# Performance work log

Hardware: AMD Instinct MI355X
Metric: run time of the kernel (lower is better)

Reference implementation:

```python
import jax, jax.numpy as jnp
import numpy as np

NU, NI, K, D, B = 100000, 50000, 100, 64, 8192


def setup_inputs() -> dict:
    key = jax.random.key(0)
    ks = jax.random.split(key, 16)
    s = lambda fan_in: np.sqrt(2.0 / fan_in)  # kaiming_normal-ish scale
    return {
        "user_emb": jax.random.normal(ks[0], (NU, D), jnp.float32) * s(D),
        "item_emb": jax.random.normal(ks[1], (NI, D), jnp.float32) * s(D),
        "user_scr_tensor": jax.random.uniform(ks[2], (NU, K), jnp.float32) / K,
        "item_scr_tensor": jax.random.uniform(ks[3], (NI, K), jnp.float32) / K,
        "w1": jax.random.normal(ks[4], (64, 128), jnp.float32) * s(128),
        "b1": jnp.zeros((64,), jnp.float32),
        "w2": jax.random.normal(ks[5], (64, 64), jnp.float32) * s(64),
        "b2": jnp.zeros((64,), jnp.float32),
        "w3": jax.random.normal(ks[6], (32, 64), jnp.float32) * s(64),
        "b3": jnp.zeros((32,), jnp.float32),
        "w4": jax.random.normal(ks[7], (32, 32), jnp.float32) * s(32),
        "b4": jnp.zeros((32,), jnp.float32),
        "w5": jax.random.normal(ks[8], (1, 32), jnp.float32) * s(32),
        "b5": jnp.zeros((1,), jnp.float32),
        "user_idx_tensor": jax.random.randint(ks[9], (NU, K), 0, NU, jnp.int32),
        "item_idx_tensor": jax.random.randint(ks[10], (NI, K), 0, NI, jnp.int32),
        "user_idxs": jax.random.randint(ks[11], (B,), 0, NU, jnp.int32),
        "item_idxs": jax.random.randint(ks[12], (B,), 0, NI, jnp.int32),
    }


def _scored_pool(idx_tensor, emb, scr, idxs):
    neighs = idx_tensor[idxs]          # [B, K]
    neigh_emb = emb[neighs]            # [B, K, D]
    neigh_scr = scr[neighs]            # [B, K, K]
    return jnp.einsum("bkj,bjd->bkd", neigh_scr, neigh_emb)


def reference(user_emb, item_emb, user_scr_tensor, item_scr_tensor,
              w1, b1, w2, b2, w3, b3, w4, b4, w5, b5,
              user_idx_tensor, item_idx_tensor, user_idxs, item_idxs):
    su = _scored_pool(user_idx_tensor, user_emb, user_scr_tensor, user_idxs)  # [B,K,D]
    si = _scored_pool(item_idx_tensor, item_emb, item_scr_tensor, item_idxs)  # [B,K,D]
    x = jnp.concatenate([su, si], axis=2)  # [B, K, 2D]
    x = jax.nn.relu(x @ w1.T + b1)
    x = jax.nn.relu(x @ w2.T + b2)
    x = jax.nn.relu(x @ w3.T + b3)
    x = jax.nn.relu(x @ w4.T + b4)
    x = jax.nn.sigmoid(x @ w5.T + b5)  # [B, K, 1]
    return jnp.mean(x, axis=-2).squeeze()  # [B]
```

## Files before the change

kernel.cpp:

```cpp
#include <hip/hip_runtime.h>
#include <hip/hip_bf16.h>
#include <math.h>

typedef __attribute__((ext_vector_type(8))) short short8;
typedef __attribute__((ext_vector_type(4))) float f32x4;

#define KN 100

#define W1_OFF 0
#define W2_OFF 8192
#define W3_OFF 12288
#define W4_OFF 14336
#define SCRU_OFF 16384
#define SCRI_OFF (SCRU_OFF + 100000 * 128)
#define EMBU_OFF (SCRI_OFF + 50000 * 128)
#define EMBI_OFF (EMBU_OFF + 100000 * 64)

#define ET_STRIDE 136
#define S_TOT (64 * ET_STRIDE)

__device__ __forceinline__ unsigned short f2bf(float f) {
  __hip_bfloat16 h = __float2bfloat16(f);
  return __builtin_bit_cast(unsigned short, h);
}

__device__ __forceinline__ void st8(unsigned short* d, float4 a, float4 b) {
  short8 h;
  h[0] = (short)f2bf(a.x); h[1] = (short)f2bf(a.y);
  h[2] = (short)f2bf(a.z); h[3] = (short)f2bf(a.w);
  h[4] = (short)f2bf(b.x); h[5] = (short)f2bf(b.y);
  h[6] = (short)f2bf(b.z); h[7] = (short)f2bf(b.w);
  *reinterpret_cast<short8*>(d) = h;
}

__device__ __forceinline__ short8 pk2(f32x4 a, f32x4 b) {
  short8 h;
  h[0] = (short)f2bf(a[0]); h[1] = (short)f2bf(a[1]);
  h[2] = (short)f2bf(a[2]); h[3] = (short)f2bf(a[3]);
  h[4] = (short)f2bf(b[0]); h[5] = (short)f2bf(b[1]);
  h[6] = (short)f2bf(b[2]); h[7] = (short)f2bf(b[3]);
  return h;
}

__global__ void prep(const float* __restrict__ w1, const float* __restrict__ w2,
                     const float* __restrict__ w3, const float* __restrict__ w4,
                     const float* __restrict__ uscr, const float* __restrict__ iscr,
                     const float* __restrict__ uemb, const float* __restrict__ iemb,
                     unsigned short* __restrict__ ws) {
  int t = blockIdx.x * 256 + threadIdx.x;
  if (t < 15360) {
    const float* src; int rel, o, i, kt, base;
    if (t < 8192)       { src = w1; rel = t;         o = rel >> 7; i = rel & 127; kt = 4; base = W1_OFF; }
    else if (t < 12288) { src = w2; rel = t - 8192;  o = rel >> 6; i = rel & 63;  kt = 2; base = W2_OFF; }
    else if (t < 14336) { src = w3; rel = t - 12288; o = rel >> 6; i = rel & 63;  kt = 2; base = W3_OFF; }
    else                { src = w4; rel = t - 14336; o = rel >> 5; i = rel & 31;  kt = 1; base = W4_OFF; }
    int n = o >> 4, l15 = o & 15, k = i >> 5;
    int quad = (i >> 2) & 3, s = ((i >> 4) & 1) * 4 + (i & 3);
    ws[base + ((n * kt + k) * 64 + quad * 16 + l15) * 8 + s] = f2bf(src[rel]);
    return;
  }
  int rel = t - 15360;
  const float4 z4 = {0.f, 0.f, 0.f, 0.f};
  if (rel < 2400000) {
    const float* src; unsigned short* dst; int row, g;
    if (rel < 1600000) {
      row = rel >> 4; g = rel & 15;
      src = uscr + (size_t)row * 100;
      dst = ws + SCRU_OFF + (size_t)row * 128 + g * 8;
    } else {
      int q = rel - 1600000; row = q >> 4; g = q & 15;
      src = iscr + (size_t)row * 100;
      dst = ws + SCRI_OFF + (size_t)row * 128 + g * 8;
    }
    const int jb = 32 * (g >> 2) + 4 * (g & 3);
    float4 va = (jb <= 96) ? *reinterpret_cast<const float4*>(src + jb) : z4;
    float4 vb = (jb <= 80) ? *reinterpret_cast<const float4*>(src + jb + 16) : z4;
    st8(dst, va, vb);
    return;
  }
  rel -= 2400000;
  if (rel < 1200000) {
    const float* src; unsigned short* dst; int row, g;
    if (rel < 800000) {
      row = rel >> 3; g = rel & 7;
      src = uemb + (size_t)row * 64;
      dst = ws + EMBU_OFF + (size_t)row * 64 + g * 8;
    } else {
      int q = rel - 800000; row = q >> 3; g = q & 7;
      src = iemb + (size_t)row * 64;
      dst = ws + EMBI_OFF + (size_t)row * 64 + g * 8;
    }
    float4 va = *reinterpret_cast<const float4*>(src + g * 8);
    float4 vb = *reinterpret_cast<const float4*>(src + g * 8 + 4);
    st8(dst, va, vb);
  }
}

__device__ __forceinline__ void pool_one(
    const unsigned short* __restrict__ scrb, const unsigned short* __restrict__ embb,
    const int* __restrict__ nb, unsigned short* __restrict__ S,
    int w, int l15, int quad, int c, int half, int mrow, bool bar_after,
    short8& f0, short8& f1) {
  short8 sb[4];
  const unsigned short* arow = scrb + (size_t)nb[mrow] * 128;
#pragma unroll
  for (int k = 0; k < 4; ++k)
    sb[k] = *reinterpret_cast<const short8*>(arow + k * 32 + quad * 8);

#pragma unroll
  for (int rr = 0; rr < 8; ++rr) {
    const int rbase = w + rr * 7;
    if (rbase < 50) {
      const int r = rbase * 2 + half;
      unsigned int v = *reinterpret_cast<const unsigned int*>(
          embb + (size_t)nb[r] * 64 + c * 2);
      const int p = 32 * (r >> 5) + 8 * ((r >> 2) & 3) + 4 * ((r >> 4) & 1) + (r & 3);
      S[(2 * c) * ET_STRIDE + p] = (unsigned short)(v & 0xffffu);
      S[(2 * c + 1) * ET_STRIDE + p] = (unsigned short)(v >> 16);
    }
  }
  __syncthreads();

  f32x4 acc[4];
#pragma unroll
  for (int po = 0; po < 4; ++po) acc[po] = (f32x4){0.f, 0.f, 0.f, 0.f};
#pragma unroll
  for (int k4 = 0; k4 < 4; ++k4) {
#pragma unroll
    for (int po = 0; po < 4; ++po) {
      short8 ea = *reinterpret_cast<const short8*>(
          S + (po * 16 + l15) * ET_STRIDE + k4 * 32 + quad * 8);
      acc[po] = __builtin_amdgcn_mfma_f32_16x16x32_bf16(ea, sb[k4], acc[po], 0, 0, 0);
    }
  }
  if (bar_after) __syncthreads();
  f0 = pk2(acc[0], acc[1]);
  f1 = pk2(acc[2], acc[3]);
}

__launch_bounds__(448)
__global__ void cnn_mfma4(
    const unsigned short* __restrict__ ws,
    const float* __restrict__ b1, const float* __restrict__ b2,
    const float* __restrict__ b3, const float* __restrict__ b4,
    const float* __restrict__ w5, const float* __restrict__ b5,
    const int* __restrict__ user_idx_t, const int* __restrict__ item_idx_t,
    const int* __restrict__ user_idxs, const int* __restrict__ item_idxs,
    float* __restrict__ out) {
  __shared__ __align__(16) unsigned short S[S_TOT];
  __shared__ int s_nb[2][112];
  __shared__ float s_red[7];

  const int b = blockIdx.x;
  const int tid = threadIdx.x;
  const int w = tid >> 6;
  const int lane = tid & 63;
  const int l15 = lane & 15, quad = lane >> 4;

  if (tid < 112) {
    s_nb[0][tid] = (tid < KN) ? user_idx_t[(size_t)user_idxs[b] * KN + tid] : 0;
  } else if (tid >= 128 && tid < 240) {
    int i = tid - 128;
    s_nb[1][i] = (i < KN) ? item_idx_t[(size_t)item_idxs[b] * KN + i] : 0;
  }
  {
    int* z = (int*)S;
    for (int i = tid; i < S_TOT / 2; i += 448) z[i] = 0;
  }
  __syncthreads();

  const int mrow = w * 16 + l15;
  const int c = lane & 31, half = lane >> 5;

  short8 x0, x1, x2, x3;
  pool_one(ws + SCRU_OFF, ws + EMBU_OFF, s_nb[0], S, w, l15, quad, c, half, mrow,
           true, x0, x1);
  pool_one(ws + SCRI_OFF, ws + EMBI_OFF, s_nb[1], S, w, l15, quad, c, half, mrow,
           false, x2, x3);

  f32x4 y[4];
#pragma unroll
  for (int po = 0; po < 4; ++po) y[po] = (f32x4){0.f, 0.f, 0.f, 0.f};
  {
    short8 xf[4] = {x0, x1, x2, x3};
#pragma unroll
    for (int k4 = 0; k4 < 4; ++k4)
#pragma unroll
      for (int po = 0; po < 4; ++po) {
        short8 wa = *reinterpret_cast<const short8*>(
            ws + W1_OFF + ((po * 4 + k4) * 64 + lane) * 8);
        y[po] = __builtin_amdgcn_mfma_f32_16x16x32_bf16(wa, xf[k4], y[po], 0, 0, 0);
      }
  }
#pragma unroll
  for (int po = 0; po < 4; ++po) {
    const float4 bb = *reinterpret_cast<const float4*>(b1 + po * 16 + quad * 4);
#pragma unroll
    for (int r = 0; r < 4; ++r) y[po][r] = fmaxf(y[po][r] + bb[r], 0.f);
  }
  short8 g0 = pk2(y[0], y[1]), g1 = pk2(y[2], y[3]);

  f32x4 v[4];
#pragma unroll
  for (int po = 0; po < 4; ++po) v[po] = (f32x4){0.f, 0.f, 0.f, 0.f};
#pragma unroll
  for (int k4 = 0; k4 < 2; ++k4) {
    short8 gf = k4 ? g1 : g0;
#pragma unroll
    for (int po = 0; po < 4; ++po) {
      short8 wa = *reinterpret_cast<const short8*>(
          ws + W2_OFF + ((po * 2 + k4) * 64 + lane) * 8);
      v[po] = __builtin_amdgcn_mfma_f32_16x16x32_bf16(wa, gf, v[po], 0, 0, 0);
    }
  }
#pragma unroll
  for (int po = 0; po < 4; ++po) {
    const float4 bb = *reinterpret_cast<const float4*>(b2 + po * 16 + quad * 4);
#pragma unroll
    for (int r = 0; r < 4; ++r) v[po][r] = fmaxf(v[po][r] + bb[r], 0.f);
  }
  short8 h0 = pk2(v[0], v[1]), h1 = pk2(v[2], v[3]);

  f32x4 t3[2];
  t3[0] = (f32x4){0.f, 0.f, 0.f, 0.f};
  t3[1] = (f32x4){0.f, 0.f, 0.f, 0.f};
#pragma unroll
  for (int k4 = 0; k4 < 2; ++k4) {
    short8 gf = k4 ? h1 : h0;
#pragma unroll
    for (int po = 0; po < 2; ++po) {
      short8 wa = *reinterpret_cast<const short8*>(
          ws + W3_OFF + ((po * 2 + k4) * 64 + lane) * 8);
      t3[po] = __builtin_amdgcn_mfma_f32_16x16x32_bf16(wa, gf, t3[po], 0, 0, 0);
    }
  }
#pragma unroll
  for (int po = 0; po < 2; ++po) {
    const float4 bb = *reinterpret_cast<const float4*>(b3 + po * 16 + quad * 4);
#pragma unroll
    for (int r = 0; r < 4; ++r) t3[po][r] = fmaxf(t3[po][r] + bb[r], 0.f);
  }
  short8 q0 = pk2(t3[0], t3[1]);

  f32x4 u[2];
  u[0] = (f32x4){0.f, 0.f, 0.f, 0.f};
  u[1] = (f32x4){0.f, 0.f, 0.f, 0.f};
#pragma unroll
  for (int po = 0; po < 2; ++po) {
    short8 wa = *reinterpret_cast<const short8*>(ws + W4_OFF + (po * 64 + lane) * 8);
    u[po] = __builtin_amdgcn_mfma_f32_16x16x32_bf16(wa, q0, u[po], 0, 0, 0);
  }
  float part = 0.f;
#pragma unroll
  for (int po = 0; po < 2; ++po) {
    const float4 bb = *reinterpret_cast<const float4*>(b4 + po * 16 + quad * 4);
    const float4 wv = *reinterpret_cast<const float4*>(w5 + po * 16 + quad * 4);
#pragma unroll
    for (int r = 0; r < 4; ++r)
      part = fmaf(fmaxf(u[po][r] + bb[r], 0.f), wv[r], part);
  }
  part += __shfl_xor(part, 16, 64);
  part += __shfl_xor(part, 32, 64);
  float sig = 1.f / (1.f + expf(-(part + b5[0])));
  if (mrow >= KN) sig = 0.f;
  sig += __shfl_xor(sig, 1, 64);
  sig += __shfl_xor(sig, 2, 64);
  sig += __shfl_xor(sig, 4, 64);
  sig += __shfl_xor(sig, 8, 64);
  if (lane == 0) s_red[w] = sig;
  __syncthreads();
  if (tid == 0) {
    float acc = 0.f;
#pragma unroll
    for (int i = 0; i < 7; ++i) acc += s_red[i];
    out[b] = acc * (1.0f / KN);
  }
}

extern "C" void kernel_launch(void* const* d_in, const int* in_sizes, int n_in,
                              void* d_out, int out_size, void* d_ws,
                              size_t ws_size, hipStream_t stream) {
  const float* user_emb = (const float*)d_in[0];
  const float* item_emb = (const float*)d_in[1];
  const float* user_scr = (const float*)d_in[2];
  const float* item_scr = (const float*)d_in[3];
  const float* w1 = (const float*)d_in[4];
  const float* b1 = (const float*)d_in[5];
  const float* w2 = (const float*)d_in[6];
  const float* b2 = (const float*)d_in[7];
  const float* w3 = (const float*)d_in[8];
  const float* b3 = (const float*)d_in[9];
  const float* w4 = (const float*)d_in[10];
  const float* b4 = (const float*)d_in[11];
  const float* w5 = (const float*)d_in[12];
  const float* b5 = (const float*)d_in[13];
  const int* user_idx_t = (const int*)d_in[14];
  const int* item_idx_t = (const int*)d_in[15];
  const int* user_idxs = (const int*)d_in[16];
  const int* item_idxs = (const int*)d_in[17];
  unsigned short* wsw = (unsigned short*)d_ws;

  prep<<<dim3((15360 + 2400000 + 1200000 + 255) / 256), dim3(256), 0, stream>>>(
      w1, w2, w3, w4, user_scr, item_scr, user_emb, item_emb, wsw);

  const int B = in_sizes[16];
  cnn_mfma4<<<dim3(B), dim3(448), 0, stream>>>(
      wsw, b1, b2, b3, b4, w5, b5, user_idx_t, item_idx_t, user_idxs,
      item_idxs, (float*)d_out);
}
```

Before: 385.3 us.

## Issue user and item gathers together with swizzled double LDS buffers

The user and item embedding and score gathers are now issued together before any LDS staging, and the two pools get separate LDS buffers, so one barrier replaces three and the second pool's global latency overlaps the first. The transpose writes pair lanes with a cross-half shuffle to store 32-bit words instead of 16-bit ones. An XOR swizzle is applied to reduce LDS bank conflicts. Launch bounds now request 4 blocks per CU, which doubles LDS use and raises register pressure from holding both sets of gathered values.

```diff
diff --git a/kernel.cpp b/kernel.cpp
--- a/kernel.cpp
+++ b/kernel.cpp
@@ -17,7 +17,9 @@
 #define EMBI_OFF (EMBU_OFF + 100000 * 64)
 
 #define ET_STRIDE 136
-#define S_TOT (64 * ET_STRIDE)
+#define ETU_OFF 0
+#define ETI_OFF (64 * ET_STRIDE)
+#define S_TOT   (2 * 64 * ET_STRIDE)
 
 __device__ __forceinline__ unsigned short f2bf(float f) {
   __hip_bfloat16 h = __float2bfloat16(f);
@@ -96,31 +98,9 @@
   }
 }
 
-__device__ __forceinline__ void pool_one(
-    const unsigned short* __restrict__ scrb, const unsigned short* __restrict__ embb,
-    const int* __restrict__ nb, unsigned short* __restrict__ S,
-    int w, int l15, int quad, int c, int half, int mrow, bool bar_after,
-    short8& f0, short8& f1) {
-  short8 sb[4];
-  const unsigned short* arow = scrb + (size_t)nb[mrow] * 128;
-#pragma unroll
-  for (int k = 0; k < 4; ++k)
-    sb[k] = *reinterpret_cast<const short8*>(arow + k * 32 + quad * 8);
-
-#pragma unroll
-  for (int rr = 0; rr < 8; ++rr) {
-    const int rbase = w + rr * 7;
-    if (rbase < 50) {
-      const int r = rbase * 2 + half;
-      unsigned int v = *reinterpret_cast<const unsigned int*>(
-          embb + (size_t)nb[r] * 64 + c * 2);
-      const int p = 32 * (r >> 5) + 8 * ((r >> 2) & 3) + 4 * ((r >> 4) & 1) + (r & 3);
-      S[(2 * c) * ET_STRIDE + p] = (unsigned short)(v & 0xffffu);
-      S[(2 * c + 1) * ET_STRIDE + p] = (unsigned short)(v >> 16);
-    }
-  }
-  __syncthreads();
-
+__device__ __forceinline__ void pool_mfma(const unsigned short* __restrict__ Sb,
+                                          const short8* sb, int l15, int quad,
+                                          short8& f0, short8& f1) {
   f32x4 acc[4];
 #pragma unroll
   for (int po = 0; po < 4; ++po) acc[po] = (f32x4){0.f, 0.f, 0.f, 0.f};
@@ -128,18 +108,18 @@
   for (int k4 = 0; k4 < 4; ++k4) {
 #pragma unroll
     for (int po = 0; po < 4; ++po) {
-      short8 ea = *reinterpret_cast<const short8*>(
-          S + (po * 16 + l15) * ET_STRIDE + k4 * 32 + quad * 8);
+      const int row = po * 16 + l15;
+      const int hw = row * ET_STRIDE + (((k4 * 4 + quad) ^ ((row >> 3) & 7)) << 3);
+      short8 ea = *reinterpret_cast<const short8*>(Sb + hw);
       acc[po] = __builtin_amdgcn_mfma_f32_16x16x32_bf16(ea, sb[k4], acc[po], 0, 0, 0);
     }
   }
-  if (bar_after) __syncthreads();
   f0 = pk2(acc[0], acc[1]);
   f1 = pk2(acc[2], acc[3]);
 }
 
-__launch_bounds__(448)
-__global__ void cnn_mfma4(
+__launch_bounds__(448, 4)
+__global__ void cnn_mfma5(
     const unsigned short* __restrict__ ws,
     const float* __restrict__ b1, const float* __restrict__ b2,
     const float* __restrict__ b3, const float* __restrict__ b4,
@@ -164,19 +144,71 @@
     s_nb[1][i] = (i < KN) ? item_idx_t[(size_t)item_idxs[b] * KN + i] : 0;
   }
   {
-    int* z = (int*)S;
-    for (int i = tid; i < S_TOT / 2; i += 448) z[i] = 0;
+    uint2* z = reinterpret_cast<uint2*>(S);
+    const uint2 z2 = {0u, 0u};
+    for (int i = tid; i < S_TOT / 4; i += 448) z[i] = z2;
   }
   __syncthreads();
 
   const int mrow = w * 16 + l15;
   const int c = lane & 31, half = lane >> 5;
+  const int* nbu = s_nb[0];
+  const int* nbi = s_nb[1];
+
+  unsigned int evu[8], evi[8];
+#pragma unroll
+  for (int rr = 0; rr < 8; ++rr) {
+    const int rbase = w + rr * 7;
+    if (rbase < 50) {
+      const int r = rbase * 2 + half;
+      evu[rr] = *reinterpret_cast<const unsigned int*>(
+          ws + EMBU_OFF + (size_t)nbu[r] * 64 + c * 2);
+      evi[rr] = *reinterpret_cast<const unsigned int*>(
+          ws + EMBI_OFF + (size_t)nbi[r] * 64 + c * 2);
+    } else {
+      evu[rr] = 0u; evi[rr] = 0u;
+    }
+  }
+  short8 sbu[4], sbi[4];
+  {
+    const unsigned short* arow = ws + SCRU_OFF + (size_t)nbu[mrow] * 128;
+#pragma unroll
+    for (int k = 0; k < 4; ++k)
+      sbu[k] = *reinterpret_cast<const short8*>(arow + k * 32 + quad * 8);
+  }
+  {
+    const unsigned short* arow = ws + SCRI_OFF + (size_t)nbi[mrow] * 128;
+#pragma unroll
+    for (int k = 0; k < 4; ++k)
+      sbi[k] = *reinterpret_cast<const short8*>(arow + k * 32 + quad * 8);
+  }
+
+#pragma unroll
+  for (int rr = 0; rr < 8; ++rr) {
+    const int rbase = w + rr * 7;
+    if (rbase < 50) {
+      const int r0 = rbase * 2;
+      const int p0 = ((r0 >> 5) << 5) | (((r0 >> 2) & 3) << 3) |
+                     (((r0 >> 4) & 1) << 2) | (r0 & 3);
+      const int sw = ((c >> 2) & 7) << 3;
+      const int q = (2 * c + half) * ET_STRIDE + (p0 ^ sw);
+      unsigned int vu = evu[rr];
+      unsigned int pu = __shfl_xor(vu, 32, 64);
+      unsigned int du = half ? ((vu & 0xffff0000u) | (pu >> 16))
+                             : ((vu & 0x0000ffffu) | (pu << 16));
+      *reinterpret_cast<unsigned int*>(&S[ETU_OFF + q]) = du;
+      unsigned int vi = evi[rr];
+      unsigned int pi = __shfl_xor(vi, 32, 64);
+      unsigned int di = half ? ((vi & 0xffff0000u) | (pi >> 16))
+                             : ((vi & 0x0000ffffu) | (pi << 16));
+      *reinterpret_cast<unsigned int*>(&S[ETI_OFF + q]) = di;
+    }
+  }
+  __syncthreads();
 
   short8 x0, x1, x2, x3;
-  pool_one(ws + SCRU_OFF, ws + EMBU_OFF, s_nb[0], S, w, l15, quad, c, half, mrow,
-           true, x0, x1);
-  pool_one(ws + SCRI_OFF, ws + EMBI_OFF, s_nb[1], S, w, l15, quad, c, half, mrow,
-           false, x2, x3);
+  pool_mfma(S + ETU_OFF, sbu, l15, quad, x0, x1);
+  pool_mfma(S + ETI_OFF, sbi, l15, quad, x2, x3);
 
   f32x4 y[4];
 #pragma unroll
@@ -304,7 +336,7 @@
       w1, w2, w3, w4, user_scr, item_scr, user_emb, item_emb, wsw);
 
   const int B = in_sizes[16];
-  cnn_mfma4<<<dim3(B), dim3(448), 0, stream>>>(
+  cnn_mfma5<<<dim3(B), dim3(448), 0, stream>>>(
       wsw, b1, b2, b3, b4, w5, b5, user_idx_t, item_idx_t, user_idxs,
       item_idxs, (float*)d_out);
 }
```

Measured after the change: 369.6 us. 1.04x faster.
